# Performance work log

Hardware: AMD Instinct MI355X
Metric: run time of the kernel (lower is better)

The kernel has to match this reference:

```python
import jax, jax.numpy as jnp
import numpy as np

N, M, K, D = 100000, 8, 256, 64  # batch, n_quantizer, n_codeword, len_subvec
LEN_VEC = M * D


def setup_inputs() -> dict:
    key = jax.random.key(0)
    k1, k2 = jax.random.split(key)
    x = jax.random.normal(k1, (N, LEN_VEC), dtype=jnp.float32)
    codebooks = jax.random.normal(k2, (M, K, D), dtype=jnp.float32)
    return {"x": x, "codebooks": codebooks, "soft_rate": -1}


def reference(x, codebooks, soft_rate):
    # x: [N, len_vec] -> [N, M, D] subvectors
    xs = x.reshape(x.shape[0], M, D)
    # squared L2 distances per (sample, quantizer, codeword): [N, M, K]
    x_sq = jnp.sum(xs * xs, axis=-1, keepdims=True)            # [N, M, 1]
    c_sq = jnp.sum(codebooks * codebooks, axis=-1)             # [M, K]
    cross = jnp.einsum('nmd,mkd->nmk', xs, codebooks)          # [N, M, K]
    dist = x_sq - 2.0 * cross + c_sq[None, :, :]               # [N, M, K]
    ids = jnp.argmin(dist, axis=-1)                            # [N, M]
    if soft_rate > 0:
        # soft assignment: convex combo of codewords weighted by softmax(-soft_rate * dist)
        w = jax.nn.softmax(-soft_rate * dist, axis=-1)         # [N, M, K]
        q = jnp.einsum('nmk,mkd->nmd', w, codebooks)           # [N, M, D]
    else:
        # hard assignment: gather nearest codeword per quantizer
        q = jnp.take_along_axis(codebooks[None], ids[:, :, None, None], axis=2)
        q = q[:, :, 0, :]                                      # [N, M, D]
    Q_x = q.reshape(-1, LEN_VEC)                               # [N, len_vec]
    id_x = ids.T.astype(jnp.int64)                             # [M, N], matches torch layout
    return Q_x, id_x
```

## Files before the change

kernel.cpp:

```cpp
#include <hip/hip_runtime.h>

#define NN 100000
#define MM 8
#define KK 256
#define DD 64
#define BROWS 128
#define NTILES ((NN + BROWS - 1) / BROWS)

typedef _Float16 half8 __attribute__((ext_vector_type(8)));
typedef float    f32x4 __attribute__((ext_vector_type(4)));


__global__ __launch_bounds__(256) void pq_prep_kernel(
    const float* __restrict__ cb, half8* __restrict__ whi,
    half8* __restrict__ wlo, float* __restrict__ csq)
{
    const int t = blockIdx.x * 256 + threadIdx.x;
    const int m = t >> 11, rest = t & 2047;
    const int c = rest >> 8, k = rest & 255;
    const float* src = cb + ((size_t)(m * KK + k)) * DD + c * 8;
    half8 h, l;
#pragma unroll
    for (int j = 0; j < 8; ++j) {
        float v = src[j];
        _Float16 hi = (_Float16)v;
        h[j] = hi;
        l[j] = (_Float16)((v - (float)hi) * 2048.0f);
    }
    whi[t] = h;
    wlo[t] = l;

    if (t < MM * KK) {
        const float* cr = cb + (size_t)t * DD;
        float s0 = 0.f, s1 = 0.f, s2 = 0.f, s3 = 0.f;
#pragma unroll
        for (int d = 0; d < DD; d += 4) {
            s0 = fmaf(cr[d + 0], cr[d + 0], s0);
            s1 = fmaf(cr[d + 1], cr[d + 1], s1);
            s2 = fmaf(cr[d + 2], cr[d + 2], s2);
            s3 = fmaf(cr[d + 3], cr[d + 3], s3);
        }
        csq[t] = (s0 + s1) + (s2 + s3);
    }
}

#define DELTA 4.0e-3f

#define MFMA16(A, B, C) __builtin_amdgcn_mfma_f32_16x16x32_f16(A, B, C, 0, 0, 0)

#define PF(P, KT)                                                          \
    {                                                                      \
        const int o_ = (KT) * 16 + ci;                                     \
        P##h0 = bh0p[o_]; P##h1 = bh1p[o_];                                \
        P##l0 = bl0p[o_]; P##l1 = bl1p[o_];                                \
    }

#define BODY(P, KT)                                                        \
    {                                                                      \
        f32x4 acc1_0 = z, acc1_1 = z, acc2_0 = z, acc2_1 = z;              \
        acc1_0 = MFMA16(Ah[0][0], P##h0, acc1_0);                          \
        acc1_0 = MFMA16(Ah[0][1], P##h1, acc1_0);                          \
        acc2_0 = MFMA16(Ah[0][0], P##l0, acc2_0);                          \
        acc2_0 = MFMA16(Ah[0][1], P##l1, acc2_0);                          \
        acc2_0 = MFMA16(Al[0][0], P##h0, acc2_0);                          \
        acc2_0 = MFMA16(Al[0][1], P##h1, acc2_0);                          \
        acc1_1 = MFMA16(Ah[1][0], P##h0, acc1_1);                          \
        acc1_1 = MFMA16(Ah[1][1], P##h1, acc1_1);                          \
        acc2_1 = MFMA16(Ah[1][0], P##l0, acc2_1);                          \
        acc2_1 = MFMA16(Ah[1][1], P##l1, acc2_1);                          \
        acc2_1 = MFMA16(Al[1][0], P##h0, acc2_1);                          \
        acc2_1 = MFMA16(Al[1][1], P##h1, acc2_1);                          \
        const int k_ = (KT) * 16 + ci;                                     \
        const float cq_ = csq_s[k_];                                       \
        _Pragma("unroll")                                                  \
        for (int r = 0; r < 4; ++r) {                                      \
            float cross0 = acc1_0[r] + acc2_0[r] * (1.0f / 2048.0f);       \
            float d0 = cq_ - 2.0f * cross0;                                \
            if (d0 < d1v[0][r]) {                                          \
                d2v[0][r] = d1v[0][r];                                     \
                d1v[0][r] = d0; k1v[0][r] = k_;                            \
            } else if (d0 < d2v[0][r]) {                                   \
                d2v[0][r] = d0;                                            \
            }                                                              \
            float cross1 = acc1_1[r] + acc2_1[r] * (1.0f / 2048.0f);       \
            float d1 = cq_ - 2.0f * cross1;                                \
            if (d1 < d1v[1][r]) {                                          \
                d2v[1][r] = d1v[1][r];                                     \
                d1v[1][r] = d1; k1v[1][r] = k_;                            \
            } else if (d1 < d2v[1][r]) {                                   \
                d2v[1][r] = d1;                                            \
            }                                                              \
        }                                                                  \
    }

__global__ __launch_bounds__(256, 3) void pq_main_kernel(
    const float* __restrict__ x, const half8* __restrict__ whi,
    const half8* __restrict__ wlo, const float* __restrict__ csqg,
    const float* __restrict__ cbf, float* __restrict__ qout,
    float* __restrict__ idout)
{
    __shared__ float csq_s[KK];
    __shared__ int   cand_k[BROWS];

    const int m   = blockIdx.y;
    const int n0  = blockIdx.x * BROWS;
    const int tid = threadIdx.x;
    const int w = tid >> 6, L = tid & 63;
    const int q = L >> 4, ci = L & 15;

    csq_s[tid] = csqg[m * KK + tid];

    half8 Ah[2][2], Al[2][2];
#pragma unroll
    for (int rb = 0; rb < 2; ++rb) {
        int n = n0 + w * 32 + rb * 16 + ci;
        if (n > NN - 1) n = NN - 1;
        const float4* xp = (const float4*)(x + (size_t)n * (MM * DD) + m * DD);
#pragma unroll
        for (int t = 0; t < 2; ++t) {
            float4 v0 = xp[t * 8 + q * 2 + 0];
            float4 v1 = xp[t * 8 + q * 2 + 1];
            float vs[8] = {v0.x, v0.y, v0.z, v0.w, v1.x, v1.y, v1.z, v1.w};
#pragma unroll
            for (int j = 0; j < 8; ++j) {
                _Float16 hi = (_Float16)vs[j];
                Ah[rb][t][j] = hi;
                Al[rb][t][j] = (_Float16)((vs[j] - (float)hi) * 2048.0f);
            }
        }
    }

    float d1v[2][4], d2v[2][4];
    int   k1v[2][4];
#pragma unroll
    for (int rb = 0; rb < 2; ++rb)
#pragma unroll
        for (int r = 0; r < 4; ++r) { d1v[rb][r] = 3.4e38f; d2v[rb][r] = 3.4e38f; k1v[rb][r] = 0; }

    const half8* bh0p = whi + m * 2048 + q * 256;
    const half8* bh1p = whi + m * 2048 + (4 + q) * 256;
    const half8* bl0p = wlo + m * 2048 + q * 256;
    const half8* bl1p = wlo + m * 2048 + (4 + q) * 256;

    __syncthreads();

    const f32x4 z = {0.f, 0.f, 0.f, 0.f};

    half8 s0h0, s0h1, s0l0, s0l1;
    half8 s1h0, s1h1, s1l0, s1l1;
    half8 s2h0, s2h1, s2l0, s2l1;

    PF(s0, 0)
    PF(s1, 1)

    PF(s2, 2)   BODY(s0, 0)
    PF(s0, 3)   BODY(s1, 1)
    PF(s1, 4)   BODY(s2, 2)
    PF(s2, 5)   BODY(s0, 3)
    PF(s0, 6)   BODY(s1, 4)
    PF(s1, 7)   BODY(s2, 5)
    PF(s2, 8)   BODY(s0, 6)
    PF(s0, 9)   BODY(s1, 7)
    PF(s1, 10)  BODY(s2, 8)
    PF(s2, 11)  BODY(s0, 9)
    PF(s0, 12)  BODY(s1, 10)
    PF(s1, 13)  BODY(s2, 11)
    PF(s2, 14)  BODY(s0, 12)
    PF(s0, 15)  BODY(s1, 13)
                BODY(s2, 14)
                BODY(s0, 15)

#pragma unroll
    for (int rb = 0; rb < 2; ++rb)
#pragma unroll
        for (int r = 0; r < 4; ++r) {
            float d = d1v[rb][r];
            int   k = k1v[rb][r];
            for (int mask = 1; mask < 16; mask <<= 1) {
                float ds = __shfl_xor(d, mask);
                int   ks = __shfl_xor(k, mask);
                if (ds < d || (ds == d && ks < k)) { d = ds; k = ks; }
            }
            const float thr = d + DELTA;
            int cnt = (d1v[rb][r] <= thr ? 1 : 0) + (d2v[rb][r] <= thr ? 1 : 0);
            for (int mask = 1; mask < 16; mask <<= 1) cnt += __shfl_xor(cnt, mask);

            const int n = n0 + w * 32 + rb * 16 + q * 4 + r;
            if (cnt > 1 && n < NN) {
                const float* xr = x + (size_t)n * (MM * DD) + m * DD;
                float s0 = 0.f, s1 = 0.f, s2 = 0.f, s3 = 0.f;
                for (int dd = 0; dd < DD; dd += 4) {
                    s0 = fmaf(xr[dd + 0], xr[dd + 0], s0);
                    s1 = fmaf(xr[dd + 1], xr[dd + 1], s1);
                    s2 = fmaf(xr[dd + 2], xr[dd + 2], s2);
                    s3 = fmaf(xr[dd + 3], xr[dd + 3], s3);
                }
                const float xsq = (s0 + s1) + (s2 + s3);
                float bd = 3.4e38f; int bk = 0;
                for (int j = 0; j < 16; ++j) {
                    const int kk = ci + 16 * j;
                    const float* c0 = cbf + ((size_t)(m * KK + kk)) * DD;
                    float a0 = 0.f, a1 = 0.f;
                    for (int dd = 0; dd < DD; dd += 2) {
                        a0 = fmaf(c0[dd + 0], xr[dd + 0], a0);
                        a1 = fmaf(c0[dd + 1], xr[dd + 1], a1);
                    }
                    const float dist = (xsq - 2.f * (a0 + a1)) + csq_s[kk];
                    if (dist < bd) { bd = dist; bk = kk; }
                }
                for (int mask = 1; mask < 16; mask <<= 1) {
                    float db = __shfl_xor(bd, mask);
                    int   kb = __shfl_xor(bk, mask);
                    if (db < bd || (db == bd && kb < bk)) { bd = db; bk = kb; }
                }
                k = bk;
            }
            if (ci == r) cand_k[w * 32 + rb * 16 + q * 4 + r] = k;
        }
    __syncthreads();

    if (tid < BROWS) {
        int n = n0 + tid;
        if (n < NN) idout[(size_t)m * NN + n] = (float)cand_k[tid];
    }
    for (int i = 0; i < 8; ++i) {
        int row = i * 16 + (tid >> 4);
        int n = n0 + row;
        if (n < NN) {
            int k = cand_k[row];
            int j = tid & 15;
            float4 v = ((const float4*)cbf)[(m * KK + k) * 16 + j];
            ((float4*)(qout + (size_t)n * (MM * DD) + m * DD))[j] = v;
        }
    }
}

extern "C" void kernel_launch(void* const* d_in, const int* in_sizes, int n_in,
                              void* d_out, int out_size, void* d_ws, size_t ws_size,
                              hipStream_t stream)
{
    const float* x  = (const float*)d_in[0];
    const float* cb = (const float*)d_in[1];

    float* qout  = (float*)d_out;
    float* idout = qout + (size_t)NN * (MM * DD);

    half8* whi = (half8*)d_ws;
    half8* wlo = (half8*)((char*)d_ws + 256 * 1024);
    float* csq = (float*)((char*)d_ws + 512 * 1024);

    pq_prep_kernel<<<dim3(64), dim3(256), 0, stream>>>(cb, whi, wlo, csq);

    pq_main_kernel<<<dim3(NTILES, MM), dim3(256), 0, stream>>>(
        x, whi, wlo, csq, cb, qout, idout);
}
```

Baseline: 428.0 us.

## Software-pipeline MFMA tiles against argmin tracking with double-buffered accumulators

After: 430.0 us. Within noise of the previous version (+0.5%).

```diff
diff --git a/kernel.cpp b/kernel.cpp
--- a/kernel.cpp
+++ b/kernel.cpp
@@ -48,33 +48,36 @@
 
 #define MFMA16(A, B, C) __builtin_amdgcn_mfma_f32_16x16x32_f16(A, B, C, 0, 0, 0)
 
-#define PF(P, KT)                                                          \
+#define PF(S, KT)                                                          \
     {                                                                      \
         const int o_ = (KT) * 16 + ci;                                     \
-        P##h0 = bh0p[o_]; P##h1 = bh1p[o_];                                \
-        P##l0 = bl0p[o_]; P##l1 = bl1p[o_];                                \
-    }
-
-#define BODY(P, KT)                                                        \
+        S##h0 = bh0p[o_]; S##h1 = bh1p[o_];                                \
+        S##l0 = bl0p[o_]; S##l1 = bl1p[o_];                                \
+    }
+
+#define MFMA_BODY(P, S)                                                    \
     {                                                                      \
-        f32x4 acc1_0 = z, acc1_1 = z, acc2_0 = z, acc2_1 = z;              \
-        acc1_0 = MFMA16(Ah[0][0], P##h0, acc1_0);                          \
-        acc1_0 = MFMA16(Ah[0][1], P##h1, acc1_0);                          \
-        acc2_0 = MFMA16(Ah[0][0], P##l0, acc2_0);                          \
-        acc2_0 = MFMA16(Ah[0][1], P##l1, acc2_0);                          \
-        acc2_0 = MFMA16(Al[0][0], P##h0, acc2_0);                          \
-        acc2_0 = MFMA16(Al[0][1], P##h1, acc2_0);                          \
-        acc1_1 = MFMA16(Ah[1][0], P##h0, acc1_1);                          \
-        acc1_1 = MFMA16(Ah[1][1], P##h1, acc1_1);                          \
-        acc2_1 = MFMA16(Ah[1][0], P##l0, acc2_1);                          \
-        acc2_1 = MFMA16(Ah[1][1], P##l1, acc2_1);                          \
-        acc2_1 = MFMA16(Al[1][0], P##h0, acc2_1);                          \
-        acc2_1 = MFMA16(Al[1][1], P##h1, acc2_1);                          \
+        P##1_0 = MFMA16(Ah[0][0], S##h0, z);                               \
+        P##1_1 = MFMA16(Ah[1][0], S##h0, z);                               \
+        P##2_0 = MFMA16(Ah[0][0], S##l0, z);                               \
+        P##2_1 = MFMA16(Ah[1][0], S##l0, z);                               \
+        P##1_0 = MFMA16(Ah[0][1], S##h1, P##1_0);                          \
+        P##1_1 = MFMA16(Ah[1][1], S##h1, P##1_1);                          \
+        P##2_0 = MFMA16(Ah[0][1], S##l1, P##2_0);                          \
+        P##2_1 = MFMA16(Ah[1][1], S##l1, P##2_1);                          \
+        P##2_0 = MFMA16(Al[0][0], S##h0, P##2_0);                          \
+        P##2_1 = MFMA16(Al[1][0], S##h0, P##2_1);                          \
+        P##2_0 = MFMA16(Al[0][1], S##h1, P##2_0);                          \
+        P##2_1 = MFMA16(Al[1][1], S##h1, P##2_1);                          \
+    }
+
+#define TRACK_BODY(P, KT)                                                  \
+    {                                                                      \
         const int k_ = (KT) * 16 + ci;                                     \
         const float cq_ = csq_s[k_];                                       \
         _Pragma("unroll")                                                  \
         for (int r = 0; r < 4; ++r) {                                      \
-            float cross0 = acc1_0[r] + acc2_0[r] * (1.0f / 2048.0f);       \
+            float cross0 = P##1_0[r] + P##2_0[r] * (1.0f / 2048.0f);       \
             float d0 = cq_ - 2.0f * cross0;                                \
             if (d0 < d1v[0][r]) {                                          \
                 d2v[0][r] = d1v[0][r];                                     \
@@ -82,7 +85,7 @@
             } else if (d0 < d2v[0][r]) {                                   \
                 d2v[0][r] = d0;                                            \
             }                                                              \
-            float cross1 = acc1_1[r] + acc2_1[r] * (1.0f / 2048.0f);       \
+            float cross1 = P##1_1[r] + P##2_1[r] * (1.0f / 2048.0f);       \
             float d1 = cq_ - 2.0f * cross1;                                \
             if (d1 < d1v[1][r]) {                                          \
                 d2v[1][r] = d1v[1][r];                                     \
@@ -146,29 +149,30 @@
 
     const f32x4 z = {0.f, 0.f, 0.f, 0.f};
 
-    half8 s0h0, s0h1, s0l0, s0l1;
-    half8 s1h0, s1h1, s1l0, s1l1;
-    half8 s2h0, s2h1, s2l0, s2l1;
-
-    PF(s0, 0)
-    PF(s1, 1)
-
-    PF(s2, 2)   BODY(s0, 0)
-    PF(s0, 3)   BODY(s1, 1)
-    PF(s1, 4)   BODY(s2, 2)
-    PF(s2, 5)   BODY(s0, 3)
-    PF(s0, 6)   BODY(s1, 4)
-    PF(s1, 7)   BODY(s2, 5)
-    PF(s2, 8)   BODY(s0, 6)
-    PF(s0, 9)   BODY(s1, 7)
-    PF(s1, 10)  BODY(s2, 8)
-    PF(s2, 11)  BODY(s0, 9)
-    PF(s0, 12)  BODY(s1, 10)
-    PF(s1, 13)  BODY(s2, 11)
-    PF(s2, 14)  BODY(s0, 12)
-    PF(s0, 15)  BODY(s1, 13)
-                BODY(s2, 14)
-                BODY(s0, 15)
+    half8 Eh0, Eh1, El0, El1;
+    half8 Oh0, Oh1, Ol0, Ol1;
+    f32x4 pa1_0, pa1_1, pa2_0, pa2_1;
+    f32x4 pb1_0, pb1_1, pb2_0, pb2_1;
+
+    PF(E, 0)
+    PF(O, 1)
+    MFMA_BODY(pa, E)
+    PF(E, 2)   MFMA_BODY(pb, O)  TRACK_BODY(pa, 0)
+    PF(O, 3)   MFMA_BODY(pa, E)  TRACK_BODY(pb, 1)
+    PF(E, 4)   MFMA_BODY(pb, O)  TRACK_BODY(pa, 2)
+    PF(O, 5)   MFMA_BODY(pa, E)  TRACK_BODY(pb, 3)
+    PF(E, 6)   MFMA_BODY(pb, O)  TRACK_BODY(pa, 4)
+    PF(O, 7)   MFMA_BODY(pa, E)  TRACK_BODY(pb, 5)
+    PF(E, 8)   MFMA_BODY(pb, O)  TRACK_BODY(pa, 6)
+    PF(O, 9)   MFMA_BODY(pa, E)  TRACK_BODY(pb, 7)
+    PF(E, 10)  MFMA_BODY(pb, O)  TRACK_BODY(pa, 8)
+    PF(O, 11)  MFMA_BODY(pa, E)  TRACK_BODY(pb, 9)
+    PF(E, 12)  MFMA_BODY(pb, O)  TRACK_BODY(pa, 10)
+    PF(O, 13)  MFMA_BODY(pa, E)  TRACK_BODY(pb, 11)
+    PF(E, 14)  MFMA_BODY(pb, O)  TRACK_BODY(pa, 12)
+    PF(O, 15)  MFMA_BODY(pa, E)  TRACK_BODY(pb, 13)
+               MFMA_BODY(pb, O)  TRACK_BODY(pa, 14)
+                                 TRACK_BODY(pb, 15)
 
 #pragma unroll
     for (int rb = 0; rb < 2; ++rb)
```
